# Kernel tuning notes

Hardware: AMD Instinct MI355X
Metric: run time of the kernel (lower is better)

Reference implementation:

```python
import jax, jax.numpy as jnp
import numpy as np

T = 256
H, W = 512, 512
SHARPNESS = 100.0
EPS = 1e-6


def setup_inputs() -> dict:
    key = jax.random.key(0)
    k1, k2 = jax.random.split(key)
    verts = jax.random.uniform(k1, (T, 3, 2), dtype=jnp.float32) * 0.5 + 0.25
    colors = jax.random.uniform(k2, (T, 3), dtype=jnp.float32)
    depth = jnp.linspace(-1.0, 1.0, T, dtype=jnp.float32)
    return {"verts": verts, "colors": colors, "depth": depth}


def _edge(px, py, va, vb):
    # va, vb: [T, 2]; px, py: [H, W] -> broadcast to [T, H, W]
    ax = va[:, 0][:, None, None]
    ay = va[:, 1][:, None, None]
    bx = vb[:, 0][:, None, None]
    by = vb[:, 1][:, None, None]
    return (px[None] - ax) * (by - ay) - (py[None] - ay) * (bx - ax)


def reference(verts, colors, depth):
    y = jnp.linspace(0.0, 1.0, H, dtype=verts.dtype)
    x = jnp.linspace(0.0, 1.0, W, dtype=verts.dtype)
    yy, xx = jnp.meshgrid(y, x, indexing="ij")  # [H, W] each

    v0 = verts[:, 0, :]  # [T, 2]
    v1 = verts[:, 1, :]
    v2 = verts[:, 2, :]

    e0 = _edge(xx, yy, v0, v1)  # [T, H, W]
    e1 = _edge(xx, yy, v1, v2)
    e2 = _edge(xx, yy, v2, v0)

    mask = (jax.nn.sigmoid(e0 * SHARPNESS)
            * jax.nn.sigmoid(e1 * SHARPNESS)
            * jax.nn.sigmoid(e2 * SHARPNESS))  # [T, H, W]

    logits = depth[:, None, None] + jnp.log(mask + EPS)  # [T, H, W]
    weights = jax.nn.softmax(logits, axis=0)             # [T, H, W]

    # composite: sum_t colors[t, c] * weights[t, h, w] -> [3, H, W]
    rgb = jnp.einsum("thw,tc->chw", weights, colors)
    return rgb
```

## Files before the change

### kernel.cpp

```cpp
#include <hip/hip_runtime.h>

#define TT 256
#define HH 512
#define WW 512
#define LOG2E 1.44269504088896340736f
#define KS (100.0f * LOG2E)
#define STEP (1.0f / 511.0f)
#define RUN 8
#define NW 8
#define CHUNK 32

__global__ __launch_bounds__(256) void tri_setup(
        const float* __restrict__ verts,
        const float* __restrict__ colors,
        const float* __restrict__ depth,
        float* __restrict__ ws) {
    int t = threadIdx.x;

    float v0x = verts[t * 6 + 0], v0y = verts[t * 6 + 1];
    float v1x = verts[t * 6 + 2], v1y = verts[t * 6 + 3];
    float v2x = verts[t * 6 + 4], v2y = verts[t * 6 + 5];

    float dx0 = v1x - v0x, dy0 = v1y - v0y;
    float dx1 = v2x - v1x, dy1 = v2y - v1y;
    float dx2 = v0x - v2x, dy2 = v0y - v2y;
    float c0 = v0y * dx0 - v0x * dy0;
    float c1 = v1y * dx1 - v1x * dy1;
    float c2 = v2y * dx2 - v2x * dy2;

    float expd = __builtin_amdgcn_exp2f(depth[t] * LOG2E);
    float cr = colors[t * 3 + 0], cg = colors[t * 3 + 1], cb = colors[t * 3 + 2];
    float ecr = expd * cr, ecg = expd * cg, ecb = expd * cb;

    float* f = ws + t * 16;
    f[0] = KS * dy0;  f[1] = KS * dx0;  f[2] = KS * c0;
    f[3] = KS * dy1;  f[4] = KS * dx1;  f[5] = KS * c1;
    f[6] = KS * dy2;  f[7] = KS * dx2;  f[8] = KS * c2;
    f[9]  = __builtin_amdgcn_exp2f(STEP * (KS * dx0));
    f[10] = __builtin_amdgcn_exp2f(STEP * (KS * dx1));
    f[11] = __builtin_amdgcn_exp2f(STEP * (KS * dx2));
    f[12] = expd; f[13] = ecr; f[14] = ecg; f[15] = ecb;

    __shared__ float4 red[256];
    red[t] = make_float4(expd * 1e-6f, ecr * 1e-6f, ecg * 1e-6f, ecb * 1e-6f);
    __syncthreads();
    for (int s = 128; s > 0; s >>= 1) {
        if (t < s) {
            float4 a = red[t], b = red[t + s];
            red[t] = make_float4(a.x + b.x, a.y + b.y, a.z + b.z, a.w + b.w);
        }
        __syncthreads();
    }
    if (t == 0) {
        ws[16 * TT + 0] = red[0].x;
        ws[16 * TT + 1] = red[0].y;
        ws[16 * TT + 2] = red[0].z;
        ws[16 * TT + 3] = red[0].w;
    }
}

__global__ __launch_bounds__(512) void tri_render(
        const float* __restrict__ ws,
        float* __restrict__ out) {
    __shared__ float4 s_part[4][RUN][64];

    int tid  = threadIdx.x;
    int lane = tid & 63;
    int wave = __builtin_amdgcn_readfirstlane(tid >> 6);

    int bx = blockIdx.x & 7;
    int by = blockIdx.x >> 3;

    float px  = (float)(bx * 64 + lane) * STEP;
    float py0 = (float)(by * RUN) * STEP;

    float acc[RUN][4];
    #pragma unroll
    for (int i = 0; i < RUN; ++i) {
        acc[i][0] = 0.0f; acc[i][1] = 0.0f; acc[i][2] = 0.0f; acc[i][3] = 0.0f;
    }

    const float* tbase = ws + wave * (CHUNK * 16);

    #pragma unroll 2
    for (int j = 0; j < CHUNK; ++j) {
        const float* tp = tbase + (j << 4);
        float Dy0 = tp[0],  Dx0 = tp[1],  C0 = tp[2];
        float Dy1 = tp[3],  Dx1 = tp[4],  C1 = tp[5];
        float Dy2 = tp[6],  Dx2 = tp[7],  C2 = tp[8];
        float k0  = tp[9],  k1  = tp[10], k2 = tp[11];
        float expd = tp[12], ecr = tp[13], ecg = tp[14], ecb = tp[15];

        float n0 = fmaf(py0, Dx0, -C0);  n0 = fmaf(-px, Dy0, n0);
        float n1 = fmaf(py0, Dx1, -C1);  n1 = fmaf(-px, Dy1, n1);
        float n2 = fmaf(py0, Dx2, -C2);  n2 = fmaf(-px, Dy2, n2);
        float u0 = __builtin_amdgcn_exp2f(n0);
        float u1 = __builtin_amdgcn_exp2f(n1);
        float u2 = __builtin_amdgcn_exp2f(n2);

        #pragma unroll
        for (int i = 0; i < RUN / 2; ++i) {
            float a  = u1 + 1.0f;
            float PA = fmaf(u0, a, a);
            PA = fmaf(u2, PA, PA);
            PA = fminf(PA, 1e18f);
            u0 *= k0; u1 *= k1; u2 *= k2;
            a = u1 + 1.0f;
            float PB = fmaf(u0, a, a);
            PB = fmaf(u2, PB, PB);
            PB = fminf(PB, 1e18f);
            if (i != RUN / 2 - 1) { u0 *= k0; u1 *= k1; u2 *= k2; }

            float rinv = __builtin_amdgcn_rcpf(PA * PB);
            float wA = rinv * PB;
            float wB = rinv * PA;

            acc[2*i][0]   = fmaf(wA, expd, acc[2*i][0]);
            acc[2*i+1][0] = fmaf(wB, expd, acc[2*i+1][0]);
            acc[2*i][1]   = fmaf(wA, ecr,  acc[2*i][1]);
            acc[2*i+1][1] = fmaf(wB, ecr,  acc[2*i+1][1]);
            acc[2*i][2]   = fmaf(wA, ecg,  acc[2*i][2]);
            acc[2*i+1][2] = fmaf(wB, ecg,  acc[2*i+1][2]);
            acc[2*i][3]   = fmaf(wA, ecb,  acc[2*i][3]);
            acc[2*i+1][3] = fmaf(wB, ecb,  acc[2*i+1][3]);
        }
    }

    if (wave >= 4) {
        #pragma unroll
        for (int i = 0; i < RUN; ++i)
            s_part[wave - 4][i][lane] =
                make_float4(acc[i][0], acc[i][1], acc[i][2], acc[i][3]);
    }
    __syncthreads();
    if (wave < 4) {
        #pragma unroll
        for (int i = 0; i < RUN; ++i) {
            float4 v = s_part[wave][i][lane];
            v.x += acc[i][0]; v.y += acc[i][1];
            v.z += acc[i][2]; v.w += acc[i][3];
            s_part[wave][i][lane] = v;
        }
    }
    __syncthreads();

    const float* base = ws + 16 * TT;
    float b0 = base[0], b1 = base[1], b2 = base[2], b3 = base[3];

    int i = tid >> 6, l = tid & 63;
    float4 v0 = s_part[0][i][l];
    float4 v1 = s_part[1][i][l];
    float4 v2 = s_part[2][i][l];
    float4 v3 = s_part[3][i][l];
    float sum = b0 + ((v0.x + v1.x) + (v2.x + v3.x));
    float r   = b1 + ((v0.y + v1.y) + (v2.y + v3.y));
    float g   = b2 + ((v0.z + v1.z) + (v2.z + v3.z));
    float bch = b3 + ((v0.w + v1.w) + (v2.w + v3.w));
    float inv = 1.0f / sum;
    int gy = by * RUN + i;
    int gx = bx * 64 + l;
    int pix = gy * WW + gx;
    out[pix]               = r   * inv;
    out[HH * WW + pix]     = g   * inv;
    out[2 * HH * WW + pix] = bch * inv;
}

extern "C" void kernel_launch(void* const* d_in, const int* in_sizes, int n_in,
                              void* d_out, int out_size, void* d_ws, size_t ws_size,
                              hipStream_t stream) {
    const float* verts  = (const float*)d_in[0];
    const float* colors = (const float*)d_in[1];
    const float* depth  = (const float*)d_in[2];
    float* out = (float*)d_out;
    float* ws  = (float*)d_ws;

    tri_setup<<<dim3(1), dim3(256), 0, stream>>>(verts, colors, depth, ws);
    tri_render<<<dim3((WW / 64) * (HH / RUN)), dim3(512), 0, stream>>>(ws, out);
}
```

Before: 34.79 us.

## Pack render inner loop into v_pk_f32 ops and skip fully-outside triangles per wave

Rewrites the per-triangle inner loop to handle two pixel rows at once with packed FP32 instructions (v_pk_fma/mul/add) through inline asm. It also adds a wave-uniform early exit that skips a triangle when every lane's largest edge exponent exceeds a threshold, meaning its weight is negligible. Launch bounds gain a minimum-blocks hint. The skip drops contributions that sit below float precision, and the asm blocks may limit compiler scheduling.

```diff
diff --git a/kernel.cpp b/kernel.cpp
--- a/kernel.cpp
+++ b/kernel.cpp
@@ -7,8 +7,25 @@
 #define KS (100.0f * LOG2E)
 #define STEP (1.0f / 511.0f)
 #define RUN 8
-#define NW 8
 #define CHUNK 32
+
+typedef float f2 __attribute__((ext_vector_type(2)));
+
+static __device__ __forceinline__ f2 pk_fma(f2 a, f2 b, f2 c) {
+    f2 d;
+    asm("v_pk_fma_f32 %0, %1, %2, %3" : "=v"(d) : "v"(a), "v"(b), "v"(c));
+    return d;
+}
+static __device__ __forceinline__ f2 pk_mul(f2 a, f2 b) {
+    f2 d;
+    asm("v_pk_mul_f32 %0, %1, %2" : "=v"(d) : "v"(a), "v"(b));
+    return d;
+}
+static __device__ __forceinline__ f2 pk_add(f2 a, f2 b) {
+    f2 d;
+    asm("v_pk_add_f32 %0, %1, %2" : "=v"(d) : "v"(a), "v"(b));
+    return d;
+}
 
 __global__ __launch_bounds__(256) void tri_setup(
         const float* __restrict__ verts,
@@ -59,7 +76,7 @@
     }
 }
 
-__global__ __launch_bounds__(512) void tri_render(
+__global__ __launch_bounds__(512, 4) void tri_render(
         const float* __restrict__ ws,
         float* __restrict__ out) {
     __shared__ float4 s_part[4][RUN][64];
@@ -74,12 +91,14 @@
     float px  = (float)(bx * 64 + lane) * STEP;
     float py0 = (float)(by * RUN) * STEP;
 
-    float acc[RUN][4];
+    f2 ACC[RUN / 2][4];
     #pragma unroll
-    for (int i = 0; i < RUN; ++i) {
-        acc[i][0] = 0.0f; acc[i][1] = 0.0f; acc[i][2] = 0.0f; acc[i][3] = 0.0f;
-    }
-
+    for (int i = 0; i < RUN / 2; ++i)
+        #pragma unroll
+        for (int c = 0; c < 4; ++c)
+            ACC[i][c] = (f2){0.0f, 0.0f};
+
+    const f2 ONES = {1.0f, 1.0f};
     const float* tbase = ws + wave * (CHUNK * 16);
 
     #pragma unroll 2
@@ -88,58 +107,77 @@
         float Dy0 = tp[0],  Dx0 = tp[1],  C0 = tp[2];
         float Dy1 = tp[3],  Dx1 = tp[4],  C1 = tp[5];
         float Dy2 = tp[6],  Dx2 = tp[7],  C2 = tp[8];
-        float k0  = tp[9],  k1  = tp[10], k2 = tp[11];
-        float expd = tp[12], ecr = tp[13], ecg = tp[14], ecb = tp[15];
 
         float n0 = fmaf(py0, Dx0, -C0);  n0 = fmaf(-px, Dy0, n0);
         float n1 = fmaf(py0, Dx1, -C1);  n1 = fmaf(-px, Dy1, n1);
         float n2 = fmaf(py0, Dx2, -C2);  n2 = fmaf(-px, Dy2, n2);
-        float u0 = __builtin_amdgcn_exp2f(n0);
-        float u1 = __builtin_amdgcn_exp2f(n1);
-        float u2 = __builtin_amdgcn_exp2f(n2);
+
+        float nmax = fmaxf(fmaxf(n0, n1), n2);
+        if (__all(nmax > 34.0f)) continue;
+
+        float k0 = tp[9], k1 = tp[10], k2 = tp[11];
+        float uA0 = __builtin_amdgcn_exp2f(n0);
+        float uA1 = __builtin_amdgcn_exp2f(n1);
+        float uA2 = __builtin_amdgcn_exp2f(n2);
+
+        f2 U0 = {uA0, uA0 * k0};
+        f2 U1 = {uA1, uA1 * k1};
+        f2 U2 = {uA2, uA2 * k2};
+        float kk0 = k0 * k0, kk1 = k1 * k1, kk2 = k2 * k2;
+        f2 K0 = {kk0, kk0};
+        f2 K1 = {kk1, kk1};
+        f2 K2 = {kk2, kk2};
+
+        float expd = tp[12], ecr = tp[13], ecg = tp[14], ecb = tp[15];
+        f2 VE = {expd, expd};
+        f2 VR = {ecr, ecr};
+        f2 VG = {ecg, ecg};
+        f2 VB = {ecb, ecb};
 
         #pragma unroll
         for (int i = 0; i < RUN / 2; ++i) {
-            float a  = u1 + 1.0f;
-            float PA = fmaf(u0, a, a);
-            PA = fmaf(u2, PA, PA);
-            PA = fminf(PA, 1e18f);
-            u0 *= k0; u1 *= k1; u2 *= k2;
-            a = u1 + 1.0f;
-            float PB = fmaf(u0, a, a);
-            PB = fmaf(u2, PB, PB);
-            PB = fminf(PB, 1e18f);
-            if (i != RUN / 2 - 1) { u0 *= k0; u1 *= k1; u2 *= k2; }
-
+            f2 A1 = pk_add(U1, ONES);
+            f2 P  = pk_fma(U0, A1, A1);
+            P     = pk_fma(U2, P, P);
+            float PA = fminf(P.x, 1e18f);
+            float PB = fminf(P.y, 1e18f);
             float rinv = __builtin_amdgcn_rcpf(PA * PB);
-            float wA = rinv * PB;
-            float wB = rinv * PA;
-
-            acc[2*i][0]   = fmaf(wA, expd, acc[2*i][0]);
-            acc[2*i+1][0] = fmaf(wB, expd, acc[2*i+1][0]);
-            acc[2*i][1]   = fmaf(wA, ecr,  acc[2*i][1]);
-            acc[2*i+1][1] = fmaf(wB, ecr,  acc[2*i+1][1]);
-            acc[2*i][2]   = fmaf(wA, ecg,  acc[2*i][2]);
-            acc[2*i+1][2] = fmaf(wB, ecg,  acc[2*i+1][2]);
-            acc[2*i][3]   = fmaf(wA, ecb,  acc[2*i][3]);
-            acc[2*i+1][3] = fmaf(wB, ecb,  acc[2*i+1][3]);
+            f2 W = {rinv * PB, rinv * PA};
+
+            ACC[i][0] = pk_fma(W, VE, ACC[i][0]);
+            ACC[i][1] = pk_fma(W, VR, ACC[i][1]);
+            ACC[i][2] = pk_fma(W, VG, ACC[i][2]);
+            ACC[i][3] = pk_fma(W, VB, ACC[i][3]);
+
+            if (i != RUN / 2 - 1) {
+                U0 = pk_mul(U0, K0);
+                U1 = pk_mul(U1, K1);
+                U2 = pk_mul(U2, K2);
+            }
         }
     }
 
     if (wave >= 4) {
         #pragma unroll
-        for (int i = 0; i < RUN; ++i)
-            s_part[wave - 4][i][lane] =
-                make_float4(acc[i][0], acc[i][1], acc[i][2], acc[i][3]);
+        for (int i = 0; i < RUN / 2; ++i) {
+            s_part[wave - 4][2 * i][lane] =
+                make_float4(ACC[i][0].x, ACC[i][1].x, ACC[i][2].x, ACC[i][3].x);
+            s_part[wave - 4][2 * i + 1][lane] =
+                make_float4(ACC[i][0].y, ACC[i][1].y, ACC[i][2].y, ACC[i][3].y);
+        }
     }
     __syncthreads();
     if (wave < 4) {
         #pragma unroll
-        for (int i = 0; i < RUN; ++i) {
-            float4 v = s_part[wave][i][lane];
-            v.x += acc[i][0]; v.y += acc[i][1];
-            v.z += acc[i][2]; v.w += acc[i][3];
-            s_part[wave][i][lane] = v;
+        for (int i = 0; i < RUN / 2; ++i) {
+            float4 v = s_part[wave][2 * i][lane];
+            v.x += ACC[i][0].x; v.y += ACC[i][1].x;
+            v.z += ACC[i][2].x; v.w += ACC[i][3].x;
+            s_part[wave][2 * i][lane] = v;
+            float4 w = s_part[wave][2 * i + 1][lane];
+            w.x += ACC[i][0].y; w.y += ACC[i][1].y;
+            w.z += ACC[i][2].y; w.w += ACC[i][3].y;
+            s_part[wave][2 * i + 1][lane] = w;
         }
     }
     __syncthreads();
```

Measured after the change: 35.99 us. +3.5%, slower.

## Skip triangles fully outside wave's pixels and split triangles across 16 waves

Applied to the files above, without the earlier changes.

Adds a wave-uniform early-out that skips a triangle when every lane's max edge exponent exceeds a threshold, meaning the mask is near zero across the pixel run. This avoids the exp, reciprocal and accumulate work for triangles that miss the tile. It also doubles the block to 1024 threads (16 waves of 16 triangles each) and widens the shared-memory reduction to match. The skip relies on the mask being negligible next to the EPS floor, which may slightly change the numerics, and the larger blocks add a deeper reduction and may lower occupancy.

```diff
diff --git a/kernel.cpp b/kernel.cpp
--- a/kernel.cpp
+++ b/kernel.cpp
@@ -7,8 +7,7 @@
 #define KS (100.0f * LOG2E)
 #define STEP (1.0f / 511.0f)
 #define RUN 8
-#define NW 8
-#define CHUNK 32
+#define CHUNK 16
 
 __global__ __launch_bounds__(256) void tri_setup(
         const float* __restrict__ verts,
@@ -59,10 +58,10 @@
     }
 }
 
-__global__ __launch_bounds__(512) void tri_render(
+__global__ __launch_bounds__(1024, 8) void tri_render(
         const float* __restrict__ ws,
         float* __restrict__ out) {
-    __shared__ float4 s_part[4][RUN][64];
+    __shared__ float4 s_part[8][RUN][64];
 
     int tid  = threadIdx.x;
     int lane = tid & 63;
@@ -88,15 +87,19 @@
         float Dy0 = tp[0],  Dx0 = tp[1],  C0 = tp[2];
         float Dy1 = tp[3],  Dx1 = tp[4],  C1 = tp[5];
         float Dy2 = tp[6],  Dx2 = tp[7],  C2 = tp[8];
-        float k0  = tp[9],  k1  = tp[10], k2 = tp[11];
-        float expd = tp[12], ecr = tp[13], ecg = tp[14], ecb = tp[15];
 
         float n0 = fmaf(py0, Dx0, -C0);  n0 = fmaf(-px, Dy0, n0);
         float n1 = fmaf(py0, Dx1, -C1);  n1 = fmaf(-px, Dy1, n1);
         float n2 = fmaf(py0, Dx2, -C2);  n2 = fmaf(-px, Dy2, n2);
+
+        float nmax = fmaxf(fmaxf(n0, n1), n2);
+        if (__all(nmax > 34.0f)) continue;
+
         float u0 = __builtin_amdgcn_exp2f(n0);
         float u1 = __builtin_amdgcn_exp2f(n1);
         float u2 = __builtin_amdgcn_exp2f(n2);
+        float k0 = tp[9], k1 = tp[10], k2 = tp[11];
+        float ce = tp[12], cr = tp[13], cg = tp[14], cb = tp[15];
 
         #pragma unroll
         for (int i = 0; i < RUN / 2; ++i) {
@@ -115,25 +118,25 @@
             float wA = rinv * PB;
             float wB = rinv * PA;
 
-            acc[2*i][0]   = fmaf(wA, expd, acc[2*i][0]);
-            acc[2*i+1][0] = fmaf(wB, expd, acc[2*i+1][0]);
-            acc[2*i][1]   = fmaf(wA, ecr,  acc[2*i][1]);
-            acc[2*i+1][1] = fmaf(wB, ecr,  acc[2*i+1][1]);
-            acc[2*i][2]   = fmaf(wA, ecg,  acc[2*i][2]);
-            acc[2*i+1][2] = fmaf(wB, ecg,  acc[2*i+1][2]);
-            acc[2*i][3]   = fmaf(wA, ecb,  acc[2*i][3]);
-            acc[2*i+1][3] = fmaf(wB, ecb,  acc[2*i+1][3]);
+            acc[2*i][0]   = fmaf(wA, ce, acc[2*i][0]);
+            acc[2*i+1][0] = fmaf(wB, ce, acc[2*i+1][0]);
+            acc[2*i][1]   = fmaf(wA, cr, acc[2*i][1]);
+            acc[2*i+1][1] = fmaf(wB, cr, acc[2*i+1][1]);
+            acc[2*i][2]   = fmaf(wA, cg, acc[2*i][2]);
+            acc[2*i+1][2] = fmaf(wB, cg, acc[2*i+1][2]);
+            acc[2*i][3]   = fmaf(wA, cb, acc[2*i][3]);
+            acc[2*i+1][3] = fmaf(wB, cb, acc[2*i+1][3]);
         }
     }
 
-    if (wave >= 4) {
+    if (wave >= 8) {
         #pragma unroll
         for (int i = 0; i < RUN; ++i)
-            s_part[wave - 4][i][lane] =
+            s_part[wave - 8][i][lane] =
                 make_float4(acc[i][0], acc[i][1], acc[i][2], acc[i][3]);
     }
     __syncthreads();
-    if (wave < 4) {
+    if (wave < 8) {
         #pragma unroll
         for (int i = 0; i < RUN; ++i) {
             float4 v = s_part[wave][i][lane];
@@ -144,25 +147,31 @@
     }
     __syncthreads();
 
-    const float* base = ws + 16 * TT;
-    float b0 = base[0], b1 = base[1], b2 = base[2], b3 = base[3];
+    if (tid < 512) {
+        const float* base = ws + 16 * TT;
+        float b0 = base[0], b1 = base[1], b2 = base[2], b3 = base[3];
 
-    int i = tid >> 6, l = tid & 63;
-    float4 v0 = s_part[0][i][l];
-    float4 v1 = s_part[1][i][l];
-    float4 v2 = s_part[2][i][l];
-    float4 v3 = s_part[3][i][l];
-    float sum = b0 + ((v0.x + v1.x) + (v2.x + v3.x));
-    float r   = b1 + ((v0.y + v1.y) + (v2.y + v3.y));
-    float g   = b2 + ((v0.z + v1.z) + (v2.z + v3.z));
-    float bch = b3 + ((v0.w + v1.w) + (v2.w + v3.w));
-    float inv = 1.0f / sum;
-    int gy = by * RUN + i;
-    int gx = bx * 64 + l;
-    int pix = gy * WW + gx;
-    out[pix]               = r   * inv;
-    out[HH * WW + pix]     = g   * inv;
-    out[2 * HH * WW + pix] = bch * inv;
+        int i = tid >> 6, l = tid & 63;
+        float4 v0 = s_part[0][i][l];
+        float4 v1 = s_part[1][i][l];
+        float4 v2 = s_part[2][i][l];
+        float4 v3 = s_part[3][i][l];
+        float4 v4 = s_part[4][i][l];
+        float4 v5 = s_part[5][i][l];
+        float4 v6 = s_part[6][i][l];
+        float4 v7 = s_part[7][i][l];
+        float sum = b0 + (((v0.x + v1.x) + (v2.x + v3.x)) + ((v4.x + v5.x) + (v6.x + v7.x)));
+        float r   = b1 + (((v0.y + v1.y) + (v2.y + v3.y)) + ((v4.y + v5.y) + (v6.y + v7.y)));
+        float g   = b2 + (((v0.z + v1.z) + (v2.z + v3.z)) + ((v4.z + v5.z) + (v6.z + v7.z)));
+        float bch = b3 + (((v0.w + v1.w) + (v2.w + v3.w)) + ((v4.w + v5.w) + (v6.w + v7.w)));
+        float inv = 1.0f / sum;
+        int gy = by * RUN + i;
+        int gx = bx * 64 + l;
+        int pix = gy * WW + gx;
+        out[pix]               = r   * inv;
+        out[HH * WW + pix]     = g   * inv;
+        out[2 * HH * WW + pix] = bch * inv;
+    }
 }
 
 extern "C" void kernel_launch(void* const* d_in, const int* in_sizes, int n_in,
@@ -175,5 +184,5 @@
     float* ws  = (float*)d_ws;
 
     tri_setup<<<dim3(1), dim3(256), 0, stream>>>(verts, colors, depth, ws);
-    tri_render<<<dim3((WW / 64) * (HH / RUN)), dim3(512), 0, stream>>>(ws, out);
+    tri_render<<<dim3((WW / 64) * (HH / RUN)), dim3(1024), 0, stream>>>(ws, out);
 }
```

After: 34.67 us. Within noise of the previous version (-0.3%).
